# Kernel optimization log

Hardware: AMD Instinct MI355X
Metric: run time of the kernel (lower is better)

The kernel has to match this reference:

```python
import jax, jax.numpy as jnp
import numpy as np

CLIP_LEN = 8      # == num_frame
NUM_NODES = 7     # == group_size
NUM_BASIC = 1024
NUM_MIXED = 8192
T = 2 * CLIP_LEN - 1          # 15 temporal offsets
N = 1 + NUM_NODES * CLIP_LEN  # 57 graph size


def setup_inputs() -> dict:
    key = jax.random.key(0)
    k1, k2, k3, k4 = jax.random.split(key, 4)
    mat = jax.random.normal(k1, (NUM_BASIC, NUM_NODES, NUM_NODES), dtype=jnp.float32)
    temp_extent = jax.random.normal(k2, (NUM_BASIC, T), dtype=jnp.float32)
    # nn.Linear(num_basic, num_mixed): weight [out,in], bias [out]
    W = jax.random.normal(k3, (NUM_MIXED, NUM_BASIC), dtype=jnp.float32) * (1.0 / np.sqrt(NUM_BASIC))
    b = jax.random.normal(k4, (NUM_MIXED,), dtype=jnp.float32) * 0.01
    return {"mat": mat, "temp_extent": temp_extent, "W": W, "b": b}


def reference(mat, temp_extent, W, b):
    n, cl = NUM_NODES, CLIP_LEN
    Hb = mat.shape[0]
    te = jax.nn.sigmoid(temp_extent) + 1.0                      # [Hb, T]
    x = jnp.einsum('ht,hnm->htmn', te, mat)                     # [Hb, T, n, n]
    x = jax.nn.relu(x)
    x = jnp.transpose(x, (1, 2, 3, 0)).reshape(T * n, n, Hb)    # (t m) n h
    y = x @ W.T + b                                             # [(t m), n, Hm]
    y = jax.nn.relu(jnp.transpose(y, (2, 1, 0)))                # [Hm, n, T*n]
    Hm = y.shape[0]
    # vectorized version of the per-frame slice-write loop:
    # frame i reads cols n*(cl-1-i) : n*(2*cl-1-i) of y
    starts = n * (cl - 1 - jnp.arange(cl))                      # [cl]
    idx = starts[:, None] + jnp.arange(n * cl)[None, :]         # [cl, n*cl]
    blocks = y[:, :, idx]                                       # [Hm, n, cl, n*cl]
    blocks = jnp.transpose(blocks, (0, 2, 1, 3)).reshape(Hm, n * cl, n * cl)
    base = jnp.zeros((Hm, N, N), dtype=y.dtype)
    base = base.at[:, 0::7, 0::7].set(1.0)                      # person-node anchors
    mixed = base.at[:, 1:, 1:].set(blocks)                      # [Hm, N, N]
    # degree normalization D^{-1/2} A D^{-1/2} (row sums, clamped at 1)
    d = jnp.clip(mixed.sum(axis=2), 1.0, None) ** -0.5          # [Hm, N]
    ret = d[:, :, None] * mixed * d[:, None, :]
    return ret
```

## Files before the change

kernel.cpp:

```cpp
#include <hip/hip_runtime.h>
#include <hip/hip_bf16.h>

#define HB 1024
#define HM 8192
#define NR 735
#define NPAD 768
#define NOUT 57

typedef __attribute__((ext_vector_type(8))) _Float16 half8;
typedef __attribute__((ext_vector_type(4))) _Float16 half4v;
typedef __attribute__((ext_vector_type(4))) float floatx4;

__global__ __launch_bounds__(256) void prep_x2_kernel(
    const float* __restrict__ mat, const float* __restrict__ tex,
    _Float16* __restrict__ Xh) {
  const int r = blockIdx.x;
  const int n = r % 7;
  const int tm = r / 7;
  const int m = tm % 7;
  const int t = tm / 7;
#pragma unroll
  for (int i = 0; i < 4; ++i) {
    const int h = i * 256 + threadIdx.x;
    float v = 0.f;
    if (r < NR) {
      const float mv = mat[h * 49 + n * 7 + m];
      const float te = 1.f / (1.f + expf(-tex[h * 15 + t])) + 1.f;
      v = te * mv;
      v = v > 0.f ? v : 0.f;
    }
    Xh[r * HB + h] = (_Float16)v;
  }
}

__global__ __launch_bounds__(256) void prep_w_kernel(
    const float4* __restrict__ W, half4v* __restrict__ Wh) {
  const int idx = blockIdx.x * 256 + threadIdx.x;
  const float4 v = W[idx];
  half4v h;
  h.x = (_Float16)v.x;
  h.y = (_Float16)v.y;
  h.z = (_Float16)v.z;
  h.w = (_Float16)v.w;
  Wh[idx] = h;
}

__global__ __launch_bounds__(256) void gemm_kernel(
    const _Float16* __restrict__ A,
    const _Float16* __restrict__ B,
    const float* __restrict__ bias,
    float* __restrict__ Y) {
  __shared__ __align__(16) _Float16 As[128 * 32];
  __shared__ __align__(16) _Float16 Bs[128 * 32];

  const int tid = threadIdx.x;
  const int lane = tid & 63;
  const int wave = tid >> 6;
  const int bm = blockIdx.x;
  const int bn = blockIdx.y;
  const int wm = (wave >> 1) * 64;
  const int wn = (wave & 1) * 64;

  floatx4 acc[4][4] = {};

  const int srow = lane >> 2;
  const int skh = (lane & 3) * 8;
  const size_t abase = (size_t)(bm * 128) * HB;
  const size_t bbase = (size_t)(bn * 128) * HB;

  const int mrow = lane & 15;
  const int quad = lane >> 4;

  for (int k0 = 0; k0 < HB; k0 += 32) {
#pragma unroll
    for (int it = 0; it < 2; ++it) {
      const int chunk = wave * 2 + it;
      const int row = chunk * 16 + srow;
      __builtin_amdgcn_global_load_lds(
          (const __attribute__((address_space(1))) void*)(A + abase + (size_t)row * HB + k0 + skh),
          (__attribute__((address_space(3))) void*)(As + chunk * 512), 16, 0, 0);
      __builtin_amdgcn_global_load_lds(
          (const __attribute__((address_space(1))) void*)(B + bbase + (size_t)row * HB + k0 + skh),
          (__attribute__((address_space(3))) void*)(Bs + chunk * 512), 16, 0, 0);
    }
    __syncthreads();

    half8 af[4], bf[4];
#pragma unroll
    for (int i = 0; i < 4; ++i) {
      af[i] = *(const half8*)(As + (wm + i * 16 + mrow) * 32 + quad * 8);
      bf[i] = *(const half8*)(Bs + (wn + i * 16 + mrow) * 32 + quad * 8);
    }
#pragma unroll
    for (int i = 0; i < 4; ++i)
#pragma unroll
      for (int j = 0; j < 4; ++j)
        acc[i][j] = __builtin_amdgcn_mfma_f32_16x16x32_f16(af[i], bf[j], acc[i][j], 0, 0, 0);
    __syncthreads();
  }

#pragma unroll
  for (int i = 0; i < 4; ++i) {
#pragma unroll
    for (int j = 0; j < 4; ++j) {
#pragma unroll
      for (int reg = 0; reg < 4; ++reg) {
        const int grow = bm * 128 + wm + i * 16 + quad * 4 + reg;
        const int gcol = bn * 128 + wn + j * 16 + mrow;
        float v = acc[i][j][reg] + bias[grow];
        v = v > 0.f ? v : 0.f;
        Y[(size_t)grow * NPAD + gcol] = v;
      }
    }
  }
}

__global__ __launch_bounds__(256) void epilogue_kernel(
    const float* __restrict__ Y, float* __restrict__ out) {
  const int j = blockIdx.x;
  __shared__ float ly[NR];
  __shared__ float dd[NOUT];

  const float* yj = Y + (size_t)j * NPAD;
  for (int i = threadIdx.x; i < NR; i += 256) ly[i] = yj[i];
  __syncthreads();

  if (threadIdx.x < NOUT) {
    const int r = threadIdx.x;
    float s;
    if (r == 0) {
      s = 9.f;
    } else {
      const int c = (r - 1) / 7;
      const int n = (r - 1) % 7;
      const int base = 7 * (7 - c);
      s = (n == 6) ? 1.f : 0.f;
#pragma unroll
      for (int p = 0; p < 56; ++p) s += ly[(base + p) * 7 + n];
    }
    s = s < 1.f ? 1.f : s;
    dd[r] = rsqrtf(s);
  }
  __syncthreads();

  float* oj = out + (size_t)j * (NOUT * NOUT);
  for (int i = threadIdx.x; i < NOUT * NOUT; i += 256) {
    const int r = i / NOUT;
    const int q = i % NOUT;
    float v;
    if (r == 0) {
      v = (q % 7 == 0) ? dd[0] * dd[q] : 0.f;
    } else {
      const int c = (r - 1) / 7;
      const int n = (r - 1) % 7;
      if (q == 0)
        v = (n == 6) ? dd[r] * dd[0] : 0.f;
      else
        v = dd[r] * ly[(7 * (7 - c) + q - 1) * 7 + n] * dd[q];
    }
    oj[i] = v;
  }
}

extern "C" void kernel_launch(void* const* d_in, const int* in_sizes, int n_in,
                              void* d_out, int out_size, void* d_ws, size_t ws_size,
                              hipStream_t stream) {
  const float* mat = (const float*)d_in[0];
  const float* tex = (const float*)d_in[1];
  const float* W = (const float*)d_in[2];
  const float* b = (const float*)d_in[3];
  float* out = (float*)d_out;

  char* ws = (char*)d_ws;
  _Float16* Xh = (_Float16*)(ws);
  _Float16* Wh = (_Float16*)(ws + (size_t)NPAD * HB * 2);
  float* Y = (float*)(ws + (size_t)NPAD * HB * 2 + (size_t)HM * HB * 2);

  prep_x2_kernel<<<NPAD, 256, 0, stream>>>(mat, tex, Xh);
  prep_w_kernel<<<HM * HB / 4 / 256, 256, 0, stream>>>((const float4*)W, (half4v*)Wh);
  gemm_kernel<<<dim3(HM / 128, NPAD / 128), 256, 0, stream>>>(Wh, Xh, b, Y);
  epilogue_kernel<<<HM, 256, 0, stream>>>(Y, out);
}
```

Measured before the change: 185.4 us.

## Split GEMM K dimension in two and fold bias/ReLU into epilogue reduction

The GEMM now splits the K=1024 reduction across two grid slices, each writing fp32 partial sums to a separate buffer, and the epilogue sums the two partials and applies bias and ReLU. The grid axes are reordered so neighbouring blocks share the same W row tile, and launch bounds request three blocks per CU. This aims to raise the block count and occupancy of the under-filled GEMM. In exchange it doubles the intermediate fp32 write traffic and the epilogue read traffic, and it needs a larger workspace.

```diff
diff --git a/kernel.cpp b/kernel.cpp
--- a/kernel.cpp
+++ b/kernel.cpp
@@ -6,6 +6,7 @@
 #define NR 735
 #define NPAD 768
 #define NOUT 57
+#define KSPLIT 2
 
 typedef __attribute__((ext_vector_type(8))) _Float16 half8;
 typedef __attribute__((ext_vector_type(4))) _Float16 half4v;
@@ -45,19 +46,19 @@
   Wh[idx] = h;
 }
 
-__global__ __launch_bounds__(256) void gemm_kernel(
+__global__ __launch_bounds__(256, 3) void gemm_kernel(
     const _Float16* __restrict__ A,
     const _Float16* __restrict__ B,
-    const float* __restrict__ bias,
-    float* __restrict__ Y) {
+    float* __restrict__ Yp) {
   __shared__ __align__(16) _Float16 As[128 * 32];
   __shared__ __align__(16) _Float16 Bs[128 * 32];
 
   const int tid = threadIdx.x;
   const int lane = tid & 63;
   const int wave = tid >> 6;
-  const int bm = blockIdx.x;
-  const int bn = blockIdx.y;
+  const int bn = blockIdx.x;
+  const int bm = blockIdx.y;
+  const int ks = blockIdx.z;
   const int wm = (wave >> 1) * 64;
   const int wn = (wave & 1) * 64;
 
@@ -71,7 +72,9 @@
   const int mrow = lane & 15;
   const int quad = lane >> 4;
 
-  for (int k0 = 0; k0 < HB; k0 += 32) {
+  const int kbeg = ks * (HB / KSPLIT);
+  const int kend = kbeg + (HB / KSPLIT);
+  for (int k0 = kbeg; k0 < kend; k0 += 32) {
 #pragma unroll
     for (int it = 0; it < 2; ++it) {
       const int chunk = wave * 2 + it;
@@ -99,6 +102,7 @@
     __syncthreads();
   }
 
+  float* Yk = Yp + (size_t)ks * HM * NPAD;
 #pragma unroll
   for (int i = 0; i < 4; ++i) {
 #pragma unroll
@@ -107,22 +111,26 @@
       for (int reg = 0; reg < 4; ++reg) {
         const int grow = bm * 128 + wm + i * 16 + quad * 4 + reg;
         const int gcol = bn * 128 + wn + j * 16 + mrow;
-        float v = acc[i][j][reg] + bias[grow];
-        v = v > 0.f ? v : 0.f;
-        Y[(size_t)grow * NPAD + gcol] = v;
+        Yk[(size_t)grow * NPAD + gcol] = acc[i][j][reg];
       }
     }
   }
 }
 
 __global__ __launch_bounds__(256) void epilogue_kernel(
-    const float* __restrict__ Y, float* __restrict__ out) {
+    const float* __restrict__ Yp, const float* __restrict__ bias,
+    float* __restrict__ out) {
   const int j = blockIdx.x;
   __shared__ float ly[NR];
   __shared__ float dd[NOUT];
 
-  const float* yj = Y + (size_t)j * NPAD;
-  for (int i = threadIdx.x; i < NR; i += 256) ly[i] = yj[i];
+  const float* y0 = Yp + (size_t)j * NPAD;
+  const float* y1 = Yp + (size_t)(HM + j) * NPAD;
+  const float bj = bias[j];
+  for (int i = threadIdx.x; i < NR; i += 256) {
+    float v = y0[i] + y1[i] + bj;
+    ly[i] = v > 0.f ? v : 0.f;
+  }
   __syncthreads();
 
   if (threadIdx.x < NOUT) {
@@ -174,10 +182,10 @@
   char* ws = (char*)d_ws;
   _Float16* Xh = (_Float16*)(ws);
   _Float16* Wh = (_Float16*)(ws + (size_t)NPAD * HB * 2);
-  float* Y = (float*)(ws + (size_t)NPAD * HB * 2 + (size_t)HM * HB * 2);
+  float* Yp = (float*)(ws + (size_t)NPAD * HB * 2 + (size_t)HM * HB * 2);
 
   prep_x2_kernel<<<NPAD, 256, 0, stream>>>(mat, tex, Xh);
   prep_w_kernel<<<HM * HB / 4 / 256, 256, 0, stream>>>((const float4*)W, (half4v*)Wh);
-  gemm_kernel<<<dim3(HM / 128, NPAD / 128), 256, 0, stream>>>(Wh, Xh, b, Y);
-  epilogue_kernel<<<HM, 256, 0, stream>>>(Y, out);
+  gemm_kernel<<<dim3(NPAD / 128, HM / 128, KSPLIT), 256, 0, stream>>>(Wh, Xh, Yp);
+  epilogue_kernel<<<HM, 256, 0, stream>>>(Yp, b, out);
 }
```

New measurement: 188.3 us. No clear change (+1.6%).

## Fuse W conversion, GEMM, and graph normalization epilogue into one kernel

Applied to the files above, without the earlier changes.

Replaces the separate W-to-fp16 conversion, GEMM, and epilogue kernels with a single kernel. Each block handles 32 output channels across all 768 columns, converts its fp32 W tile to fp16 inline, and double-buffers the LDS stages. The block then keeps the ReLU'd GEMM result in shared memory and computes the degree normalization and the 57x57 output there. This avoids the fp16 W copy and the Y intermediate round-trips through global memory. In exchange it uses about 100 KB of LDS per block with one block per CU, launches only 256 blocks, and re-reads the whole X matrix for every block.

```diff
diff --git a/kernel.cpp b/kernel.cpp
--- a/kernel.cpp
+++ b/kernel.cpp
@@ -6,6 +6,8 @@
 #define NR 735
 #define NPAD 768
 #define NOUT 57
+#define BM 32
+#define YS 736
 
 typedef __attribute__((ext_vector_type(8))) _Float16 half8;
 typedef __attribute__((ext_vector_type(4))) _Float16 half4v;
@@ -33,100 +35,104 @@
   }
 }
 
-__global__ __launch_bounds__(256) void prep_w_kernel(
-    const float4* __restrict__ W, half4v* __restrict__ Wh) {
-  const int idx = blockIdx.x * 256 + threadIdx.x;
-  const float4 v = W[idx];
-  half4v h;
-  h.x = (_Float16)v.x;
-  h.y = (_Float16)v.y;
-  h.z = (_Float16)v.z;
-  h.w = (_Float16)v.w;
-  Wh[idx] = h;
-}
-
-__global__ __launch_bounds__(256) void gemm_kernel(
-    const _Float16* __restrict__ A,
-    const _Float16* __restrict__ B,
+__global__ __launch_bounds__(256, 1) void fused_kernel(
+    const float* __restrict__ W,
+    const _Float16* __restrict__ Xh,
     const float* __restrict__ bias,
-    float* __restrict__ Y) {
-  __shared__ __align__(16) _Float16 As[128 * 32];
-  __shared__ __align__(16) _Float16 Bs[128 * 32];
+    float* __restrict__ out) {
+  extern __shared__ char smem[];
+  _Float16* const As0 = (_Float16*)smem;
+  _Float16* const As1 = (_Float16*)(smem + 2048);
+  _Float16* const Bs0 = (_Float16*)(smem + 4096);
+  _Float16* const Bs1 = (_Float16*)(smem + 53248);
+  float* const ly = (float*)smem;
+  float* const dd = (float*)(smem + 94208);
 
   const int tid = threadIdx.x;
   const int lane = tid & 63;
   const int wave = tid >> 6;
-  const int bm = blockIdx.x;
-  const int bn = blockIdx.y;
-  const int wm = (wave >> 1) * 64;
-  const int wn = (wave & 1) * 64;
-
-  floatx4 acc[4][4] = {};
-
-  const int srow = lane >> 2;
-  const int skh = (lane & 3) * 8;
-  const size_t abase = (size_t)(bm * 128) * HB;
-  const size_t bbase = (size_t)(bn * 128) * HB;
-
-  const int mrow = lane & 15;
+  const int j0 = blockIdx.x * BM;
+  const int row16 = lane & 15;
   const int quad = lane >> 4;
 
-  for (int k0 = 0; k0 < HB; k0 += 32) {
+  floatx4 acc[2][12] = {};
+
+  const int arow = tid >> 3;
+  const int acol = (tid & 7) * 4;
+  const float* const Wrow = W + (size_t)(j0 + arow) * HB + acol;
+
+  const int brow = lane >> 2;
+  const int bkoff = (lane & 3) * 8;
+
+  auto stage = [&](int k0, _Float16* Asb, _Float16* Bsb) {
 #pragma unroll
-    for (int it = 0; it < 2; ++it) {
-      const int chunk = wave * 2 + it;
-      const int row = chunk * 16 + srow;
+    for (int cc = 0; cc < 12; ++cc) {
+      const int c = wave * 12 + cc;
+      const int row = c * 16 + brow;
       __builtin_amdgcn_global_load_lds(
-          (const __attribute__((address_space(1))) void*)(A + abase + (size_t)row * HB + k0 + skh),
-          (__attribute__((address_space(3))) void*)(As + chunk * 512), 16, 0, 0);
-      __builtin_amdgcn_global_load_lds(
-          (const __attribute__((address_space(1))) void*)(B + bbase + (size_t)row * HB + k0 + skh),
-          (__attribute__((address_space(3))) void*)(Bs + chunk * 512), 16, 0, 0);
+          (const __attribute__((address_space(1))) void*)(Xh + (size_t)row * HB + k0 + bkoff),
+          (__attribute__((address_space(3))) void*)(Bsb + c * 512), 16, 0, 0);
     }
+    const float4 w4 = *(const float4*)(Wrow + k0);
+    half4v h4;
+    h4.x = (_Float16)w4.x;
+    h4.y = (_Float16)w4.y;
+    h4.z = (_Float16)w4.z;
+    h4.w = (_Float16)w4.w;
+    *(half4v*)(Asb + arow * 32 + acol) = h4;
+  };
+
+  stage(0, As0, Bs0);
+  for (int k = 0; k < HB / 32; ++k) {
+    const int cur = k & 1;
+    _Float16* const Asc = cur ? As1 : As0;
+    _Float16* const Bsc = cur ? Bs1 : Bs0;
+    if (k + 1 < HB / 32) stage((k + 1) * 32, cur ? As0 : As1, cur ? Bs0 : Bs1);
     __syncthreads();
 
-    half8 af[4], bf[4];
+    half8 af[2], bf[12];
 #pragma unroll
-    for (int i = 0; i < 4; ++i) {
-      af[i] = *(const half8*)(As + (wm + i * 16 + mrow) * 32 + quad * 8);
-      bf[i] = *(const half8*)(Bs + (wn + i * 16 + mrow) * 32 + quad * 8);
-    }
+    for (int i = 0; i < 2; ++i)
+      af[i] = *(const half8*)(Asc + (i * 16 + row16) * 32 + quad * 8);
 #pragma unroll
-    for (int i = 0; i < 4; ++i)
+    for (int jt = 0; jt < 12; ++jt)
+      bf[jt] = *(const half8*)(Bsc + (wave * 192 + jt * 16 + row16) * 32 + quad * 8);
 #pragma unroll
-      for (int j = 0; j < 4; ++j)
-        acc[i][j] = __builtin_amdgcn_mfma_f32_16x16x32_f16(af[i], bf[j], acc[i][j], 0, 0, 0);
+    for (int i = 0; i < 2; ++i)
+#pragma unroll
+      for (int jt = 0; jt < 12; ++jt)
+        acc[i][jt] = __builtin_amdgcn_mfma_f32_16x16x32_f16(af[i], bf[jt], acc[i][jt], 0, 0, 0);
     __syncthreads();
   }
 
+  float bv[2][4];
 #pragma unroll
-  for (int i = 0; i < 4; ++i) {
+  for (int i = 0; i < 2; ++i)
 #pragma unroll
-    for (int j = 0; j < 4; ++j) {
+    for (int reg = 0; reg < 4; ++reg)
+      bv[i][reg] = bias[j0 + i * 16 + quad * 4 + reg];
+
 #pragma unroll
-      for (int reg = 0; reg < 4; ++reg) {
-        const int grow = bm * 128 + wm + i * 16 + quad * 4 + reg;
-        const int gcol = bn * 128 + wn + j * 16 + mrow;
-        float v = acc[i][j][reg] + bias[grow];
-        v = v > 0.f ? v : 0.f;
-        Y[(size_t)grow * NPAD + gcol] = v;
+  for (int i = 0; i < 2; ++i) {
+#pragma unroll
+    for (int jt = 0; jt < 12; ++jt) {
+      const int col = wave * 192 + jt * 16 + row16;
+      if (col < YS) {
+#pragma unroll
+        for (int reg = 0; reg < 4; ++reg) {
+          const int row = i * 16 + quad * 4 + reg;
+          float v = acc[i][jt][reg] + bv[i][reg];
+          ly[row * YS + col] = v > 0.f ? v : 0.f;
+        }
       }
     }
   }
-}
-
-__global__ __launch_bounds__(256) void epilogue_kernel(
-    const float* __restrict__ Y, float* __restrict__ out) {
-  const int j = blockIdx.x;
-  __shared__ float ly[NR];
-  __shared__ float dd[NOUT];
-
-  const float* yj = Y + (size_t)j * NPAD;
-  for (int i = threadIdx.x; i < NR; i += 256) ly[i] = yj[i];
   __syncthreads();
 
-  if (threadIdx.x < NOUT) {
-    const int r = threadIdx.x;
+  for (int idx = tid; idx < BM * NOUT; idx += 256) {
+    const int jj = idx / NOUT;
+    const int r = idx % NOUT;
+    const float* lyj = ly + jj * YS;
     float s;
     if (r == 0) {
       s = 9.f;
@@ -136,29 +142,40 @@
       const int base = 7 * (7 - c);
       s = (n == 6) ? 1.f : 0.f;
 #pragma unroll
-      for (int p = 0; p < 56; ++p) s += ly[(base + p) * 7 + n];
+      for (int p = 0; p < 56; ++p) s += lyj[(base + p) * 7 + n];
     }
     s = s < 1.f ? 1.f : s;
-    dd[r] = rsqrtf(s);
+    dd[idx] = rsqrtf(s);
   }
   __syncthreads();
 
-  float* oj = out + (size_t)j * (NOUT * NOUT);
-  for (int i = threadIdx.x; i < NOUT * NOUT; i += 256) {
-    const int r = i / NOUT;
-    const int q = i % NOUT;
-    float v;
-    if (r == 0) {
-      v = (q % 7 == 0) ? dd[0] * dd[q] : 0.f;
-    } else {
-      const int c = (r - 1) / 7;
-      const int n = (r - 1) % 7;
-      if (q == 0)
-        v = (n == 6) ? dd[r] * dd[0] : 0.f;
-      else
-        v = dd[r] * ly[(7 * (7 - c) + q - 1) * 7 + n] * dd[q];
+  float4* const o4 = (float4*)(out + (size_t)j0 * (NOUT * NOUT));
+  const int total4 = BM * NOUT * NOUT / 4;
+  for (int idx = tid; idx < total4; idx += 256) {
+    float4 v4;
+#pragma unroll
+    for (int e = 0; e < 4; ++e) {
+      const int g = idx * 4 + e;
+      const int jj = g / (NOUT * NOUT);
+      const int i = g % (NOUT * NOUT);
+      const int r = i / NOUT;
+      const int q = i % NOUT;
+      const float* lyj = ly + jj * YS;
+      const float* ddj = dd + jj * NOUT;
+      float v;
+      if (r == 0) {
+        v = (q % 7 == 0) ? ddj[0] * ddj[q] : 0.f;
+      } else {
+        const int c = (r - 1) / 7;
+        const int n = (r - 1) % 7;
+        if (q == 0)
+          v = (n == 6) ? ddj[r] * ddj[0] : 0.f;
+        else
+          v = ddj[r] * lyj[(7 * (7 - c) + q - 1) * 7 + n] * ddj[q];
+      }
+      ((float*)&v4)[e] = v;
     }
-    oj[i] = v;
+    o4[idx] = v4;
   }
 }
 
@@ -171,13 +188,8 @@
   const float* b = (const float*)d_in[3];
   float* out = (float*)d_out;
 
-  char* ws = (char*)d_ws;
-  _Float16* Xh = (_Float16*)(ws);
-  _Float16* Wh = (_Float16*)(ws + (size_t)NPAD * HB * 2);
-  float* Y = (float*)(ws + (size_t)NPAD * HB * 2 + (size_t)HM * HB * 2);
+  _Float16* Xh = (_Float16*)d_ws;
 
   prep_x2_kernel<<<NPAD, 256, 0, stream>>>(mat, tex, Xh);
-  prep_w_kernel<<<HM * HB / 4 / 256, 256, 0, stream>>>((const float4*)W, (half4v*)Wh);
-  gemm_kernel<<<dim3(HM / 128, NPAD / 128), 256, 0, stream>>>(Wh, Xh, b, Y);
-  epilogue_kernel<<<HM, 256, 0, stream>>>(Y, out);
+  fused_kernel<<<HM / BM, 256, 102400, stream>>>(W, Xh, b, out);
 }
```

Measured after the change: 267.2 us. +44.1%, slower.
